# Kernel optimization log

Measured on AMD Instinct MI355X. Metric: run time of the kernel, lower is better.

Reference implementation:

```python
import jax, jax.numpy as jnp
import numpy as np

L = 24
D = 2048
NUM_BLOCKS = 8
EPS = 1e-6
B, T = 2, 1024


def _block_layout(num_layers, num_blocks):
    base = num_layers // num_blocks
    rem = num_layers % num_blocks
    sizes = [base] * num_blocks
    if rem:
        sizes[-1] += rem
    starts = list(np.cumsum([0] + sizes[:-1]))
    return sizes, starts


def _rmsnorm(x, weight, eps=EPS):
    # x: (..., d)
    var = jnp.mean(x * x, axis=-1, keepdims=True)
    return x * jax.lax.rsqrt(var + eps) * weight


def setup_inputs() -> dict:
    key = jax.random.key(0)
    k1, k2, k3 = jax.random.split(key, 3)
    layer_outputs = jax.random.normal(k1, (L, B, T, D), dtype=jnp.float32)
    embedding = jax.random.normal(k2, (B, T, D), dtype=jnp.float32)
    queries = jax.random.normal(k3, (L, D), dtype=jnp.float32) * 0.02
    key_norm_weight = jnp.ones((D,), dtype=jnp.float32)
    return {
        "layer_outputs": layer_outputs,
        "embedding": embedding,
        "queries": queries,
        "key_norm_weight": key_norm_weight,
    }


def reference(layer_outputs, embedding, queries, key_norm_weight):
    """Faithful port of BlockAttnRes.compute_all_inputs.

    layer_outputs: (L, B, T, d)  -- f_l(h_l) for each layer
    embedding:     (B, T, d)     -- b_0
    queries:       (L, d)        -- zero-init pseudo-queries (randn here)
    key_norm_weight: (d,)        -- RMSNorm scale
    Returns (L, B, T, d): AttnRes input h_l for each layer.
    """
    num_layers = layer_outputs.shape[0]
    sizes, starts = _block_layout(num_layers, NUM_BLOCKS)

    block_reprs = [embedding]
    partial = None
    inputs = []
    block_n = 0
    for l in range(num_layers):  # fixed structural loop over layers
        # advance block index
        while l >= starts[block_n] + sizes[block_n]:
            block_n += 1
        i = l - starts[block_n]
        sources = list(block_reprs)
        if i > 0 and partial is not None:
            sources.append(partial)
        v_stack = jnp.stack(sources, axis=2)            # (B, T, n, d)
        k_stack = _rmsnorm(v_stack, key_norm_weight)    # (B, T, n, d)
        scores = jnp.einsum("btnd,d->btn", k_stack, queries[l])
        alpha = jax.nn.softmax(scores, axis=-1)         # (B, T, n)
        h = jnp.einsum("btn,btnd->btd", alpha, v_stack)
        inputs.append(h)
        f_l = layer_outputs[l]
        partial = f_l if partial is None else partial + f_l
        if i + 1 >= sizes[block_n]:
            block_reprs.append(partial)
            partial = None
    return jnp.stack(inputs, axis=0)  # (L, B, T, d)
```

## Files before the change

### kernel.cpp

```cpp
#include <hip/hip_runtime.h>
#include <hip/hip_bf16.h>

constexpr int LAYERS = 24;
constexpr int DIM    = 2048;
constexpr int NBLK   = 8;
constexpr float EPSV = 1e-6f;
constexpr int TPB    = 512;
constexpr int EPT    = 4;
constexpr int NSLOT  = 147;
constexpr int RSTR   = NSLOT + 2;

typedef float vf4 __attribute__((ext_vector_type(4)));

__device__ constexpr int OFF_TAB[24] =
    {0,1,4,7,10,14,18,22,27,32,37,43,49,55,62,69,76,84,92,100,109,118,127,137};

__device__ __forceinline__ unsigned pk2(float a, float b) {
    __hip_bfloat162 h2(__float2bfloat16(a), __float2bfloat16(b));
    union { __hip_bfloat162 h; unsigned u; } c; c.h = h2; return c.u;
}
__device__ __forceinline__ float upk(unsigned p, int hi) {
    union { unsigned u; float f; } c;
    c.u = hi ? (p & 0xffff0000u) : (p << 16);
    return c.f;
}

template<int CTRL>
__device__ __forceinline__ float dpp_nbor(float x) {
    int y = __builtin_amdgcn_update_dpp(0, __float_as_int(x), CTRL, 0xF, 0xF, true);
    return __int_as_float(y);
}
__device__ __forceinline__ float grp16_sum(float x) {
    x += dpp_nbor<0xB1>(x);
    x += dpp_nbor<0x4E>(x);
    x += dpp_nbor<0x141>(x);
    x += dpp_nbor<0x140>(x);
    return x;
}
__device__ __forceinline__ float grp16_max(float x) {
    x = fmaxf(x, dpp_nbor<0xB1>(x));
    x = fmaxf(x, dpp_nbor<0x4E>(x));
    x = fmaxf(x, dpp_nbor<0x141>(x));
    x = fmaxf(x, dpp_nbor<0x140>(x));
    return x;
}

__global__ void __launch_bounds__(TPB, 4)
block_attn_res_kernel(const float* __restrict__ lo,
                      const float* __restrict__ emb,
                      const float* __restrict__ qry,
                      const float* __restrict__ wgt,
                      float* __restrict__ out,
                      int bt_total)
{
    const int bt   = blockIdx.x;
    const int tid  = threadIdx.x;
    const int lane = tid & 63;
    const int wid  = tid >> 6;
    const int grp  = (wid << 2) | (lane >> 4);
    const int c0   = tid * 4;

    __shared__ float red[32][RSTR];
    __shared__ float ab[LAYERS][12];

    const float invD = 1.f / (float)DIM;
    const size_t lstride = (size_t)bt_total * DIM;
    const float* lop = lo + (size_t)bt * DIM + c0;

    auto wred = [&](float x, int slot) {
        x = grp16_sum(x);
        if ((lane & 15) == 0) red[grp][slot] = x;
    };

    float wv[EPT];
    {
        vf4 w0 = *reinterpret_cast<const vf4*>(wgt + c0);
        wv[0]=w0.x; wv[1]=w0.y; wv[2]=w0.z; wv[3]=w0.w;
    }

    float e[EPT];
    {
        vf4 v0 = __builtin_nontemporal_load(
            reinterpret_cast<const vf4*>(emb + (size_t)bt * DIM + c0));
        e[0]=v0.x; e[1]=v0.y; e[2]=v0.z; e[3]=v0.w;
    }

    unsigned pp[16][EPT/2];
    unsigned Spk[NBLK-1][EPT/2];
    float part[EPT];

    auto emit = [&](int l) {
        const int m = l / 3;
        const int i = l - 3 * m;
        float h[EPT];
        {
            const float a0 = ab[l][0];
            #pragma unroll
            for (int j = 0; j < EPT; ++j) h[j] = a0 * e[j];
        }
        #pragma unroll
        for (int s = 0; s < NBLK - 1; ++s) {
            if (s < m) {
                const float a = ab[l][1 + s];
                h[0] += a * upk(Spk[s][0],0);
                h[1] += a * upk(Spk[s][0],1);
                h[2] += a * upk(Spk[s][1],0);
                h[3] += a * upk(Spk[s][1],1);
            }
        }
        if (i > 0) {
            const float a = ab[l][1 + m];
            const int si = 2 * m + (i - 1);
            h[0] += a * upk(pp[si][0],0);
            h[1] += a * upk(pp[si][0],1);
            h[2] += a * upk(pp[si][1],0);
            h[3] += a * upk(pp[si][1],1);
        }
        vf4 w0; w0.x=h[0]; w0.y=h[1]; w0.z=h[2]; w0.w=h[3];
        *reinterpret_cast<vf4*>(out + ((size_t)l * bt_total + bt) * DIM + c0) = w0;
    };

    float fb[4][EPT], qb[4][EPT];
    auto p1_body = [&](int l) {
        const int m   = l / 3;
        const int i   = l - 3 * m;
        const int off = OFF_TAB[l];
        const int pf  = l & 3;

        float qwv[EPT];
        #pragma unroll
        for (int j = 0; j < EPT; ++j) qwv[j] = qb[pf][j] * wv[j];
        float fC[EPT];
        if (l < LAYERS - 1) {
            #pragma unroll
            for (int j = 0; j < EPT; ++j) fC[j] = fb[pf][j];
        }

        if (l + 4 <= LAYERS - 1) {
            vf4 v0 = *reinterpret_cast<const vf4*>(qry + (size_t)(l + 4) * DIM + c0);
            qb[pf][0]=v0.x; qb[pf][1]=v0.y; qb[pf][2]=v0.z; qb[pf][3]=v0.w;
        }
        if (l + 4 <= LAYERS - 2) {
            vf4 u0 = __builtin_nontemporal_load(
                reinterpret_cast<const vf4*>(lop + (size_t)(l + 4) * lstride));
            fb[pf][0]=u0.x; fb[pf][1]=u0.y; fb[pf][2]=u0.z; fb[pf][3]=u0.w;
        }

        {
            float dv = e[0]*qwv[0] + e[1]*qwv[1] + e[2]*qwv[2] + e[3]*qwv[3];
            wred(dv, off);
        }
        #pragma unroll
        for (int s = 0; s < NBLK - 1; ++s) {
            if (s < m) {
                float dv;
                if (s == m - 1 && i == 0) {
                    dv = part[0]*qwv[0] + part[1]*qwv[1]
                       + part[2]*qwv[2] + part[3]*qwv[3];
                } else {
                    dv = upk(Spk[s][0],0)*qwv[0] + upk(Spk[s][0],1)*qwv[1]
                       + upk(Spk[s][1],0)*qwv[2] + upk(Spk[s][1],1)*qwv[3];
                }
                wred(dv, off + 1 + s);
            }
        }
        if (i > 0) {
            float dv = part[0]*qwv[0] + part[1]*qwv[1]
                     + part[2]*qwv[2] + part[3]*qwv[3];
            float sq = part[0]*part[0] + part[1]*part[1]
                     + part[2]*part[2] + part[3]*part[3];
            wred(dv, off + m + 1);
            wred(sq, off + m + 2);
            const int si = 2 * m + (i - 1);
            pp[si][0] = pk2(part[0], part[1]);
            pp[si][1] = pk2(part[2], part[3]);
        } else {
            float sq = part[0]*part[0] + part[1]*part[1]
                     + part[2]*part[2] + part[3]*part[3];
            wred(sq, off + m + 1);
        }

        if (l < LAYERS - 1) {
            if (i == 0) {
                #pragma unroll
                for (int j = 0; j < EPT; ++j) part[j] = fC[j];
            } else {
                #pragma unroll
                for (int j = 0; j < EPT; ++j) part[j] += fC[j];
            }
            if (i == 2 && m < NBLK - 1) {
                Spk[m][0] = pk2(part[0], part[1]);
                Spk[m][1] = pk2(part[2], part[3]);
            }
        }
    };

    auto grp_softmax = [&](int gl, int gh) {
        const int l = grp;
        if (l >= gl && l <= gh) {
            const int s = lane & 15;
            const int m = l / 3;
            const int i = l - 3 * m;
            const int nsrc = 1 + m + (i > 0 ? 1 : 0);
            const int n = l - 1;
            const int t = n / 3;
            const int f = 3 * t * (t - 1) / 2 + (n % 3 + 1) * t;
            const int off = 1 + 2 * n + f + n - n / 3;
            const bool act = (s < nsrc);
            int dotslot = act ? off + s : 0;
            int ssqslot = 0;
            if (act && s > 0)
                ssqslot = (s <= m) ? (9 * s + 3 * s * (s - 1) / 2) : (off + s + 1);
            float dot = 0.f, sq = 0.f;
            #pragma unroll
            for (int g = 0; g < 32; ++g) {
                dot += red[g][dotslot];
                sq  += red[g][ssqslot];
            }
            float sc = act ? dot * rsqrtf(sq * invD + EPSV) : -3.0e38f;
            const float mx = grp16_max(sc);
            const float ee = act ? __expf(sc - mx) : 0.f;
            const float den = grp16_sum(ee);
            if (act) ab[l][s] = ee / den;
        }
    };

    {
        vf4 u0 = __builtin_nontemporal_load(reinterpret_cast<const vf4*>(lop));
        part[0]=u0.x; part[1]=u0.y; part[2]=u0.z; part[3]=u0.w;

        vf4 w0; w0.x=e[0]; w0.y=e[1]; w0.z=e[2]; w0.w=e[3];
        *reinterpret_cast<vf4*>(out + (size_t)bt * DIM + c0) = w0;

        float sq = e[0]*e[0] + e[1]*e[1] + e[2]*e[2] + e[3]*e[3];
        wred(sq, 0);
    }
    {
        #pragma unroll
        for (int k = 1; k <= 4; ++k) {
            vf4 q = *reinterpret_cast<const vf4*>(qry + (size_t)k * DIM + c0);
            qb[k & 3][0]=q.x; qb[k & 3][1]=q.y; qb[k & 3][2]=q.z; qb[k & 3][3]=q.w;
            vf4 u = __builtin_nontemporal_load(
                reinterpret_cast<const vf4*>(lop + (size_t)k * lstride));
            fb[k & 3][0]=u.x; fb[k & 3][1]=u.y; fb[k & 3][2]=u.z; fb[k & 3][3]=u.w;
        }
    }
    #pragma unroll
    for (int l = 1; l <= 7; ++l) p1_body(l);

    __syncthreads();
    grp_softmax(1, 7);
    __syncthreads();

    #pragma unroll
    for (int l = 8; l <= 15; ++l) {
        p1_body(l);
        if (l <= 14) emit(l - 7);
    }

    __syncthreads();
    grp_softmax(8, 15);
    __syncthreads();

    #pragma unroll
    for (int l = 16; l <= 23; ++l) {
        p1_body(l);
        emit(l - 8);
    }

    __syncthreads();
    grp_softmax(16, 23);
    __syncthreads();

    #pragma unroll
    for (int l = 16; l <= 23; ++l) emit(l);
}

extern "C" void kernel_launch(void* const* d_in, const int* in_sizes, int n_in,
                              void* d_out, int out_size, void* d_ws, size_t ws_size,
                              hipStream_t stream) {
    const float* lo  = (const float*)d_in[0];
    const float* emb = (const float*)d_in[1];
    const float* qry = (const float*)d_in[2];
    const float* wgt = (const float*)d_in[3];
    float* outp = (float*)d_out;

    const int bt_total = in_sizes[1] / DIM;

    block_attn_res_kernel<<<bt_total, TPB, 0, stream>>>(
        lo, emb, qry, wgt, outp, bt_total);
}
```

Baseline: 176.4 us.

## Premultiply queries by norm weight in prep kernel and deepen prefetch to six

Adds a small prep kernel that multiplies the queries by the RMSNorm weight into workspace, so the main kernel skips the weight load and the per-layer multiply. The register prefetch ring for queries and layer outputs grows from four to six layers ahead, to hide more global memory latency. The cost is an extra kernel launch and more registers per thread, which may lower occupancy under the launch bounds.

```diff
diff --git a/kernel.cpp b/kernel.cpp
--- a/kernel.cpp
+++ b/kernel.cpp
@@ -9,6 +9,7 @@
 constexpr int EPT    = 4;
 constexpr int NSLOT  = 147;
 constexpr int RSTR   = NSLOT + 2;
+constexpr int PD     = 6;
 
 typedef float vf4 __attribute__((ext_vector_type(4)));
 
@@ -45,10 +46,18 @@
     return x;
 }
 
+__global__ void prep_qw_kernel(const float* __restrict__ q,
+                               const float* __restrict__ w,
+                               float* __restrict__ qw, int n) {
+    int idx = blockIdx.x * blockDim.x + threadIdx.x;
+    if (idx < n) qw[idx] = q[idx] * w[idx & (DIM - 1)];
+}
+
+template<bool PREMUL>
 __global__ void __launch_bounds__(TPB, 4)
 block_attn_res_kernel(const float* __restrict__ lo,
                       const float* __restrict__ emb,
-                      const float* __restrict__ qry,
+                      const float* __restrict__ q1,
                       const float* __restrict__ wgt,
                       float* __restrict__ out,
                       int bt_total)
@@ -73,7 +82,7 @@
     };
 
     float wv[EPT];
-    {
+    if (!PREMUL) {
         vf4 w0 = *reinterpret_cast<const vf4*>(wgt + c0);
         wv[0]=w0.x; wv[1]=w0.y; wv[2]=w0.z; wv[3]=w0.w;
     }
@@ -120,29 +129,30 @@
         *reinterpret_cast<vf4*>(out + ((size_t)l * bt_total + bt) * DIM + c0) = w0;
     };
 
-    float fb[4][EPT], qb[4][EPT];
+    float fb[PD][EPT], qb[PD][EPT];
     auto p1_body = [&](int l) {
         const int m   = l / 3;
         const int i   = l - 3 * m;
         const int off = OFF_TAB[l];
-        const int pf  = l & 3;
+        const int pf  = l % PD;
 
         float qwv[EPT];
         #pragma unroll
-        for (int j = 0; j < EPT; ++j) qwv[j] = qb[pf][j] * wv[j];
+        for (int j = 0; j < EPT; ++j)
+            qwv[j] = PREMUL ? qb[pf][j] : qb[pf][j] * wv[j];
         float fC[EPT];
         if (l < LAYERS - 1) {
             #pragma unroll
             for (int j = 0; j < EPT; ++j) fC[j] = fb[pf][j];
         }
 
-        if (l + 4 <= LAYERS - 1) {
-            vf4 v0 = *reinterpret_cast<const vf4*>(qry + (size_t)(l + 4) * DIM + c0);
+        if (l + PD <= LAYERS - 1) {
+            vf4 v0 = *reinterpret_cast<const vf4*>(q1 + (size_t)(l + PD) * DIM + c0);
             qb[pf][0]=v0.x; qb[pf][1]=v0.y; qb[pf][2]=v0.z; qb[pf][3]=v0.w;
         }
-        if (l + 4 <= LAYERS - 2) {
+        if (l + PD <= LAYERS - 2) {
             vf4 u0 = __builtin_nontemporal_load(
-                reinterpret_cast<const vf4*>(lop + (size_t)(l + 4) * lstride));
+                reinterpret_cast<const vf4*>(lop + (size_t)(l + PD) * lstride));
             fb[pf][0]=u0.x; fb[pf][1]=u0.y; fb[pf][2]=u0.z; fb[pf][3]=u0.w;
         }
 
@@ -237,12 +247,12 @@
     }
     {
         #pragma unroll
-        for (int k = 1; k <= 4; ++k) {
-            vf4 q = *reinterpret_cast<const vf4*>(qry + (size_t)k * DIM + c0);
-            qb[k & 3][0]=q.x; qb[k & 3][1]=q.y; qb[k & 3][2]=q.z; qb[k & 3][3]=q.w;
+        for (int k = 1; k <= PD; ++k) {
+            vf4 q = *reinterpret_cast<const vf4*>(q1 + (size_t)k * DIM + c0);
+            qb[k % PD][0]=q.x; qb[k % PD][1]=q.y; qb[k % PD][2]=q.z; qb[k % PD][3]=q.w;
             vf4 u = __builtin_nontemporal_load(
                 reinterpret_cast<const vf4*>(lop + (size_t)k * lstride));
-            fb[k & 3][0]=u.x; fb[k & 3][1]=u.y; fb[k & 3][2]=u.z; fb[k & 3][3]=u.w;
+            fb[k % PD][0]=u.x; fb[k % PD][1]=u.y; fb[k % PD][2]=u.z; fb[k % PD][3]=u.w;
         }
     }
     #pragma unroll
@@ -286,7 +296,15 @@
     float* outp = (float*)d_out;
 
     const int bt_total = in_sizes[1] / DIM;
-
-    block_attn_res_kernel<<<bt_total, TPB, 0, stream>>>(
-        lo, emb, qry, wgt, outp, bt_total);
-}
+    const int nq = in_sizes[2];
+
+    if (ws_size >= (size_t)nq * sizeof(float)) {
+        float* qwbuf = (float*)d_ws;
+        prep_qw_kernel<<<(nq + 255) / 256, 256, 0, stream>>>(qry, wgt, qwbuf, nq);
+        block_attn_res_kernel<true><<<bt_total, TPB, 0, stream>>>(
+            lo, emb, qwbuf, nullptr, outp, bt_total);
+    } else {
+        block_attn_res_kernel<false><<<bt_total, TPB, 0, stream>>>(
+            lo, emb, qry, wgt, outp, bt_total);
+    }
+}
```

After: 181.5 us. 2.9% more time.
